# Kernel tuning notes

Hardware: AMD Instinct MI355X
Metric: run time of the kernel (lower is better)

Reference implementation:

```python
import jax, jax.numpy as jnp
import numpy as np

N = 131072

def setup_inputs() -> dict:
    key = jax.random.key(0)
    k_x, k_e, k_w2, k_b2, k_w3, k_b3, k_w4 = jax.random.split(key, 7)
    x = jax.random.randint(k_x, (N, 32), 0, 7424, dtype=jnp.int32)
    emb = jax.random.normal(k_e, (7424, 128), dtype=jnp.float32) * 0.05
    W2 = jax.random.normal(k_w2, (32, 128), dtype=jnp.float32) * 0.05
    b2 = jax.random.normal(k_b2, (32,), dtype=jnp.float32) * 0.05
    W3 = jax.random.normal(k_w3, (32, 64), dtype=jnp.float32) * 0.05
    b3 = jax.random.normal(k_b3, (32,), dtype=jnp.float32) * 0.05
    W4 = jax.random.normal(k_w4, (1, 64), dtype=jnp.float32) * 0.05
    return {"x": x, "emb": emb, "W2": W2, "b2": b2, "W3": W3, "b3": b3, "W4": W4}

def reference(x, emb, W2, b2, W3, b3, W4):
    # x: [N, 32] int indices; use first 29 slots
    idx = x[..., :29]
    h = emb[idx].sum(axis=-2)                    # [N, 128] embedding-bag sum
    h = jax.nn.relu(h)
    h = h @ W2.T + b2                            # [N, 32]
    h = jax.nn.relu(jnp.concatenate((h, -h), axis=-1))   # [N, 64] sign-concat
    h = h @ W3.T + b3                            # [N, 32]
    h = jax.nn.relu(jnp.concatenate((h, -h), axis=-1))   # [N, 64]
    return h @ W4.T                              # [N, 1] (no bias)
```

## Files before the change

kernel.cpp:

```cpp
#include <hip/hip_runtime.h>
#include <hip/hip_fp16.h>


typedef _Float16 h2v_t  __attribute__((ext_vector_type(2)));
typedef _Float16 half8  __attribute__((ext_vector_type(8)));
typedef float    f32x4  __attribute__((ext_vector_type(4)));

constexpr int RPB = 64;

__global__ __launch_bounds__(256) void emb_to_fp16(
    const float* __restrict__ emb, __half2* __restrict__ emb16,
    int npairs_real, int npairs_tot)
{
    int i = blockIdx.x * blockDim.x + threadIdx.x;
    if (i < npairs_tot) {
        float2 v = make_float2(0.f, 0.f);
        if (i < npairs_real) v = ((const float2*)emb)[i];
        emb16[i] = __floats2half2_rn(v.x, v.y);
    }
}

__global__ __launch_bounds__(256) void w_to_fp16(
    const float* __restrict__ W2, const float* __restrict__ W3,
    _Float16* __restrict__ W2h, _Float16* __restrict__ W3h)
{
    int i = blockIdx.x * blockDim.x + threadIdx.x;
    if (i < 4096) W2h[i] = (_Float16)W2[i];
    if (i < 2048) W3h[i] = (_Float16)W3[i];
}

__global__ __launch_bounds__(256, 8) void gather_kernel(
    const int*    __restrict__ x,
    const __half* __restrict__ emb16,
    uint4*        __restrict__ hout,
    int n)
{
    __shared__ int xlds[4][512];

    const int tid  = threadIdx.x;
    const int lane = tid & 63;
    const int wave = tid >> 6;
    const int row0 = blockIdx.x * RPB;
    const int wrow0 = __builtin_amdgcn_readfirstlane(row0 + wave * 16);

    const int g   = lane >> 4;
    const int sub = lane & 15;
    const unsigned subOff = (unsigned)sub * 16u;

    {
        const int4* xb = (const int4*)(x + (size_t)wrow0 * 32);
        int4 a = xb[lane * 2];
        int4 b = xb[lane * 2 + 1];
        if ((lane & 3) == 3) { b.y = 7424; b.z = 7424; b.w = 7424; }
        ((int4*)&xlds[wave][0])[lane * 2]     = a;
        ((int4*)&xlds[wave][0])[lane * 2 + 1] = b;
    }

    #pragma unroll 4
    for (int r = 0; r < 16; ++r) {
        const int* xrow = &xlds[wave][r * 32 + g];
        uint4 v[8];
        #pragma unroll
        for (int b = 0; b < 8; ++b) {
            const int idx = xrow[4 * b];
            const unsigned off = ((unsigned)idx << 8) + subOff;
            v[b] = *(const uint4*)((const char*)emb16 + off);
        }
        h2v_t hacc[4];
        #pragma unroll
        for (int q = 0; q < 4; ++q) hacc[q] = (h2v_t)0;
        #pragma unroll
        for (int b = 0; b < 8; ++b) {
            hacc[0] += __builtin_bit_cast(h2v_t, v[b].x);
            hacc[1] += __builtin_bit_cast(h2v_t, v[b].y);
            hacc[2] += __builtin_bit_cast(h2v_t, v[b].z);
            hacc[3] += __builtin_bit_cast(h2v_t, v[b].w);
        }
        #pragma unroll
        for (int q = 0; q < 4; ++q) {
            unsigned u = __builtin_bit_cast(unsigned, hacc[q]);
            h2v_t t = __builtin_bit_cast(h2v_t, u);
            t += __builtin_bit_cast(h2v_t, (unsigned)__shfl_xor((int)u, 16));
            unsigned u2 = __builtin_bit_cast(unsigned, t);
            t += __builtin_bit_cast(h2v_t, (unsigned)__shfl_xor((int)u2, 32));
            hacc[q] = __builtin_elementwise_max(t, (h2v_t)0);
        }
        if (g == 0) {
            const int row = wrow0 + r;
            if (row < n) {
                uint4 o;
                o.x = __builtin_bit_cast(unsigned, hacc[0]);
                o.y = __builtin_bit_cast(unsigned, hacc[1]);
                o.z = __builtin_bit_cast(unsigned, hacc[2]);
                o.w = __builtin_bit_cast(unsigned, hacc[3]);
                hout[(size_t)row * 16 + sub] = o;
            }
        }
    }
}

__global__ __launch_bounds__(256) void dense_mfma(
    const uint4*    __restrict__ hbuf,
    const _Float16* __restrict__ W2h,
    const _Float16* __restrict__ W3h,
    const float*    __restrict__ b2,
    const float*    __restrict__ b3,
    const float*    __restrict__ W4,
    float*          __restrict__ out, int n)
{
    __shared__ _Float16 a2lds[4][16 * 68];

    const int tid  = threadIdx.x;
    const int lane = tid & 63;
    const int wave = tid >> 6;
    const int q    = lane >> 4;
    const int nn   = lane & 15;
    const int row0 = blockIdx.x * 64 + wave * 16;

    half8 bw2[2][4];
    #pragma unroll
    for (int nt = 0; nt < 2; ++nt)
        #pragma unroll
        for (int kk = 0; kk < 4; ++kk)
            bw2[nt][kk] = __builtin_bit_cast(half8,
                *(const uint4*)((const char*)W2h +
                    ((nt * 16 + nn) * 128 + kk * 32 + q * 8) * 2));

    const int rowm = min(row0 + nn, n - 1);
    const char* hb = (const char*)hbuf + (size_t)rowm * 256;
    half8 af[4];
    #pragma unroll
    for (int kk = 0; kk < 4; ++kk)
        af[kk] = __builtin_bit_cast(half8,
            *(const uint4*)(hb + kk * 64 + q * 16));

    f32x4 acc0 = {0.f, 0.f, 0.f, 0.f}, acc1 = {0.f, 0.f, 0.f, 0.f};
    #pragma unroll
    for (int kk = 0; kk < 4; ++kk) {
        acc0 = __builtin_amdgcn_mfma_f32_16x16x32_f16(af[kk], bw2[0][kk], acc0, 0, 0, 0);
        acc1 = __builtin_amdgcn_mfma_f32_16x16x32_f16(af[kk], bw2[1][kk], acc1, 0, 0, 0);
    }
    const float bb0 = b2[nn], bb1 = b2[16 + nn];

    _Float16* a2 = &a2lds[wave][0];
    #pragma unroll
    for (int r = 0; r < 4; ++r) {
        const float v0 = acc0[r] + bb0;
        const float v1 = acc1[r] + bb1;
        const int m = q * 4 + r;
        a2[m * 68 + nn]      = (_Float16)fmaxf(v0, 0.f);
        a2[m * 68 + 16 + nn] = (_Float16)fmaxf(v1, 0.f);
        a2[m * 68 + 32 + nn] = (_Float16)fmaxf(-v0, 0.f);
        a2[m * 68 + 48 + nn] = (_Float16)fmaxf(-v1, 0.f);
    }

    half8 bw3[2][2];
    #pragma unroll
    for (int nt = 0; nt < 2; ++nt)
        #pragma unroll
        for (int kk = 0; kk < 2; ++kk)
            bw3[nt][kk] = __builtin_bit_cast(half8,
                *(const uint4*)((const char*)W3h +
                    ((nt * 16 + nn) * 64 + kk * 32 + q * 8) * 2));

    half8 a2f[2];
    #pragma unroll
    for (int kk = 0; kk < 2; ++kk) {
        const _Float16* p = &a2[nn * 68 + kk * 32 + q * 8];
        half8 t;
        #pragma unroll
        for (int j = 0; j < 8; ++j) t[j] = p[j];
        a2f[kk] = t;
    }

    f32x4 acc30 = {0.f, 0.f, 0.f, 0.f}, acc31 = {0.f, 0.f, 0.f, 0.f};
    #pragma unroll
    for (int kk = 0; kk < 2; ++kk) {
        acc30 = __builtin_amdgcn_mfma_f32_16x16x32_f16(a2f[kk], bw3[0][kk], acc30, 0, 0, 0);
        acc31 = __builtin_amdgcn_mfma_f32_16x16x32_f16(a2f[kk], bw3[1][kk], acc31, 0, 0, 0);
    }
    const float bb30 = b3[nn], bb31 = b3[16 + nn];

    const float w4a = W4[nn],      w4b = W4[16 + nn];
    const float w4c = W4[32 + nn], w4d = W4[48 + nn];
    float o[4];
    #pragma unroll
    for (int r = 0; r < 4; ++r) {
        const float v0 = acc30[r] + bb30;
        const float v1 = acc31[r] + bb31;
        o[r] = fmaxf(v0, 0.f) * w4a + fmaxf(-v0, 0.f) * w4c
             + fmaxf(v1, 0.f) * w4b + fmaxf(-v1, 0.f) * w4d;
    }
    #pragma unroll
    for (int s = 1; s < 16; s <<= 1) {
        #pragma unroll
        for (int r = 0; r < 4; ++r) o[r] += __shfl_xor(o[r], s);
    }
    if (nn == 0) {
        #pragma unroll
        for (int r = 0; r < 4; ++r) {
            const int row = row0 + q * 4 + r;
            if (row < n) out[row] = o[r];
        }
    }
}

__global__ __launch_bounds__(256) void nnue_fused(
    const int*    __restrict__ x,
    const __half* __restrict__ emb16,
    const float*  __restrict__ W2, const float* __restrict__ b2,
    const float*  __restrict__ W3, const float* __restrict__ b3,
    const float*  __restrict__ W4,
    float*        __restrict__ out, int n)
{
    __shared__ int     xlds[4][512];
    __shared__ __half2 hbuf[64][65];
    __shared__ float   h2T[32 * 64];
    __shared__ float   obuf[4][64];

    const int tid  = threadIdx.x;
    const int lane = tid & 63;
    const int wave = tid >> 6;
    const int row0 = blockIdx.x * RPB;
    const int wrow0 = __builtin_amdgcn_readfirstlane(row0 + wave * 16);
    const int g   = lane >> 4;
    const int sub = lane & 15;
    const unsigned subOff = (unsigned)sub * 16u;

    {
        const int4* xb = (const int4*)(x + (size_t)wrow0 * 32);
        int4 a = xb[lane * 2];
        int4 b = xb[lane * 2 + 1];
        if ((lane & 3) == 3) { b.y = 7424; b.z = 7424; b.w = 7424; }
        ((int4*)&xlds[wave][0])[lane * 2]     = a;
        ((int4*)&xlds[wave][0])[lane * 2 + 1] = b;
    }

    #pragma unroll 4
    for (int r = 0; r < 16; ++r) {
        const int* xrow = &xlds[wave][r * 32 + g];
        uint4 v[8];
        #pragma unroll
        for (int b = 0; b < 8; ++b) {
            const int idx = xrow[4 * b];
            const unsigned off = ((unsigned)idx << 8) + subOff;
            v[b] = *(const uint4*)((const char*)emb16 + off);
        }
        h2v_t hacc[4];
        #pragma unroll
        for (int q = 0; q < 4; ++q) hacc[q] = (h2v_t)0;
        #pragma unroll
        for (int b = 0; b < 8; ++b) {
            hacc[0] += __builtin_bit_cast(h2v_t, v[b].x);
            hacc[1] += __builtin_bit_cast(h2v_t, v[b].y);
            hacc[2] += __builtin_bit_cast(h2v_t, v[b].z);
            hacc[3] += __builtin_bit_cast(h2v_t, v[b].w);
        }
        #pragma unroll
        for (int q = 0; q < 4; ++q) {
            unsigned u = __builtin_bit_cast(unsigned, hacc[q]);
            h2v_t t = __builtin_bit_cast(h2v_t, u);
            t += __builtin_bit_cast(h2v_t, (unsigned)__shfl_xor((int)u, 16));
            unsigned u2 = __builtin_bit_cast(unsigned, t);
            t += __builtin_bit_cast(h2v_t, (unsigned)__shfl_xor((int)u2, 32));
            hacc[q] = __builtin_elementwise_max(t, (h2v_t)0);
        }
        if (g == 0) {
            const int row = wave * 16 + r;
            #pragma unroll
            for (int q = 0; q < 4; ++q)
                hbuf[row][sub * 4 + q] = __builtin_bit_cast(__half2, hacc[q]);
        }
    }
    __syncthreads();

    {
        const int j0 = wave * 8;
        const int rr = lane;
        float acc[8];
        #pragma unroll
        for (int j = 0; j < 8; ++j) acc[j] = b2[j0 + j];
        #pragma unroll
        for (int d2 = 0; d2 < 64; ++d2) {
            const __half2 hv = hbuf[rr][d2];
            const float vx = __low2float(hv), vy = __high2float(hv);
            #pragma unroll
            for (int j = 0; j < 8; ++j) {
                const float* w = W2 + (size_t)(j0 + j) * 128 + d2 * 2;
                acc[j] = fmaf(vx, w[0], acc[j]);
                acc[j] = fmaf(vy, w[1], acc[j]);
            }
        }
        #pragma unroll
        for (int j = 0; j < 8; ++j) h2T[(j0 + j) * 64 + rr] = acc[j];
    }
    __syncthreads();

    {
        const int j0 = wave * 8;
        const int rr = lane;
        float h2v[32];
        #pragma unroll
        for (int k = 0; k < 32; ++k) h2v[k] = h2T[k * 64 + rr];
        float acc[8];
        #pragma unroll
        for (int j = 0; j < 8; ++j) acc[j] = b3[j0 + j];
        #pragma unroll
        for (int k = 0; k < 32; ++k) {
            const float p = fmaxf(h2v[k], 0.f);
            const float m = fmaxf(-h2v[k], 0.f);
            #pragma unroll
            for (int j = 0; j < 8; ++j) {
                const float* w = W3 + (size_t)(j0 + j) * 64;
                acc[j] = fmaf(p, w[k],      acc[j]);
                acc[j] = fmaf(m, w[32 + k], acc[j]);
            }
        }
        float o = 0.f;
        #pragma unroll
        for (int j = 0; j < 8; ++j) {
            const int jj = j0 + j;
            o = fmaf(fmaxf(acc[j], 0.f),  W4[jj],      o);
            o = fmaf(fmaxf(-acc[j], 0.f), W4[32 + jj], o);
        }
        obuf[wave][rr] = o;
    }
    __syncthreads();

    if (tid < 64) {
        const int row = row0 + tid;
        if (row < n)
            out[row] = obuf[0][tid] + obuf[1][tid] + obuf[2][tid] + obuf[3][tid];
    }
}

extern "C" void kernel_launch(void* const* d_in, const int* in_sizes, int n_in,
                              void* d_out, int out_size, void* d_ws, size_t ws_size,
                              hipStream_t stream) {
    const int*   x   = (const int*)  d_in[0];
    const float* emb = (const float*)d_in[1];
    const float* W2  = (const float*)d_in[2];
    const float* b2  = (const float*)d_in[3];
    const float* W3  = (const float*)d_in[4];
    const float* b3  = (const float*)d_in[5];
    const float* W4  = (const float*)d_in[6];
    float* out = (float*)d_out;
    const int n = out_size;

    __half2* emb16 = (__half2*)d_ws;
    const int npairs_real = 7424 * 64;
    const int npairs_tot  = 7425 * 64;
    hipLaunchKernelGGL(emb_to_fp16, dim3((npairs_tot + 255) / 256), dim3(256),
                       0, stream, emb, emb16, npairs_real, npairs_tot);

    const size_t emb_bytes = (size_t)7425 * 256;
    const size_t w2h_off   = emb_bytes;
    const size_t w3h_off   = w2h_off + 8192;
    const size_t h_off     = w3h_off + 4096;
    const size_t h_bytes   = (size_t)n * 256;
    const bool   split_ok  = ws_size >= h_off + h_bytes;

    if (split_ok) {
        _Float16* W2h = (_Float16*)((char*)d_ws + w2h_off);
        _Float16* W3h = (_Float16*)((char*)d_ws + w3h_off);
        uint4*    hb  = (uint4*)   ((char*)d_ws + h_off);
        hipLaunchKernelGGL(w_to_fp16, dim3(16), dim3(256), 0, stream,
                           W2, W3, W2h, W3h);
        hipLaunchKernelGGL(gather_kernel, dim3((n + RPB - 1) / RPB), dim3(256),
                           0, stream, x, (const __half*)emb16, hb, n);
        hipLaunchKernelGGL(dense_mfma, dim3((n + 63) / 64), dim3(256),
                           0, stream, (const uint4*)hb, W2h, W3h, b2, b3, W4,
                           out, n);
    } else {
        hipLaunchKernelGGL(nnue_fused, dim3((n + RPB - 1) / RPB), dim3(256),
                           0, stream, x, (const __half*)emb16, W2, b2, W3, b3,
                           W4, out, n);
    }
}
```

Baseline: 131.9 us.

## Fuse embedding gather and MFMA dense layers into one kernel via LDS

Merges the gather kernel and the dense MFMA kernel into a single kernel. Each wave keeps its 16 pooled fp16 rows in a padded LDS tile and feeds them straight to the MFMA layers, so the N×256-byte intermediate buffer is never written to or read back from global memory, and one launch is removed. The index scratch space is reused for the second-layer activations. Occupancy drops from 8 to 6 blocks per CU, and the dense phase now sits in the same kernel as the latency-bound gather, which may hurt overlap.

```diff
diff --git a/kernel.cpp b/kernel.cpp
--- a/kernel.cpp
+++ b/kernel.cpp
@@ -29,13 +29,18 @@
     if (i < 2048) W3h[i] = (_Float16)W3[i];
 }
 
-__global__ __launch_bounds__(256, 8) void gather_kernel(
-    const int*    __restrict__ x,
-    const __half* __restrict__ emb16,
-    uint4*        __restrict__ hout,
-    int n)
+__global__ __launch_bounds__(256, 6) void nnue_one(
+    const int*      __restrict__ x,
+    const __half*   __restrict__ emb16,
+    const _Float16* __restrict__ W2h,
+    const _Float16* __restrict__ W3h,
+    const float*    __restrict__ b2,
+    const float*    __restrict__ b3,
+    const float*    __restrict__ W4,
+    float*          __restrict__ out, int n)
 {
-    __shared__ int xlds[4][512];
+    __shared__ uint4 hT[4][16 * 17];
+    __shared__ __align__(16) char scratch[4][2176];
 
     const int tid  = threadIdx.x;
     const int lane = tid & 63;
@@ -47,18 +52,20 @@
     const int sub = lane & 15;
     const unsigned subOff = (unsigned)sub * 16u;
 
+    int* xw = (int*)&scratch[wave][0];
+
     {
         const int4* xb = (const int4*)(x + (size_t)wrow0 * 32);
         int4 a = xb[lane * 2];
         int4 b = xb[lane * 2 + 1];
         if ((lane & 3) == 3) { b.y = 7424; b.z = 7424; b.w = 7424; }
-        ((int4*)&xlds[wave][0])[lane * 2]     = a;
-        ((int4*)&xlds[wave][0])[lane * 2 + 1] = b;
+        ((int4*)xw)[lane * 2]     = a;
+        ((int4*)xw)[lane * 2 + 1] = b;
     }
 
     #pragma unroll 4
     for (int r = 0; r < 16; ++r) {
-        const int* xrow = &xlds[wave][r * 32 + g];
+        const int* xrow = &xw[r * 32 + g];
         uint4 v[8];
         #pragma unroll
         for (int b = 0; b < 8; ++b) {
@@ -86,36 +93,17 @@
             hacc[q] = __builtin_elementwise_max(t, (h2v_t)0);
         }
         if (g == 0) {
-            const int row = wrow0 + r;
-            if (row < n) {
-                uint4 o;
-                o.x = __builtin_bit_cast(unsigned, hacc[0]);
-                o.y = __builtin_bit_cast(unsigned, hacc[1]);
-                o.z = __builtin_bit_cast(unsigned, hacc[2]);
-                o.w = __builtin_bit_cast(unsigned, hacc[3]);
-                hout[(size_t)row * 16 + sub] = o;
-            }
-        }
-    }
-}
-
-__global__ __launch_bounds__(256) void dense_mfma(
-    const uint4*    __restrict__ hbuf,
-    const _Float16* __restrict__ W2h,
-    const _Float16* __restrict__ W3h,
-    const float*    __restrict__ b2,
-    const float*    __restrict__ b3,
-    const float*    __restrict__ W4,
-    float*          __restrict__ out, int n)
-{
-    __shared__ _Float16 a2lds[4][16 * 68];
-
-    const int tid  = threadIdx.x;
-    const int lane = tid & 63;
-    const int wave = tid >> 6;
-    const int q    = lane >> 4;
-    const int nn   = lane & 15;
-    const int row0 = blockIdx.x * 64 + wave * 16;
+            uint4 o;
+            o.x = __builtin_bit_cast(unsigned, hacc[0]);
+            o.y = __builtin_bit_cast(unsigned, hacc[1]);
+            o.z = __builtin_bit_cast(unsigned, hacc[2]);
+            o.w = __builtin_bit_cast(unsigned, hacc[3]);
+            hT[wave][r * 17 + sub] = o;
+        }
+    }
+
+    const int q  = lane >> 4;
+    const int nn = lane & 15;
 
     half8 bw2[2][4];
     #pragma unroll
@@ -126,13 +114,10 @@
                 *(const uint4*)((const char*)W2h +
                     ((nt * 16 + nn) * 128 + kk * 32 + q * 8) * 2));
 
-    const int rowm = min(row0 + nn, n - 1);
-    const char* hb = (const char*)hbuf + (size_t)rowm * 256;
     half8 af[4];
     #pragma unroll
     for (int kk = 0; kk < 4; ++kk)
-        af[kk] = __builtin_bit_cast(half8,
-            *(const uint4*)(hb + kk * 64 + q * 16));
+        af[kk] = __builtin_bit_cast(half8, hT[wave][nn * 17 + (4 * kk + q)]);
 
     f32x4 acc0 = {0.f, 0.f, 0.f, 0.f}, acc1 = {0.f, 0.f, 0.f, 0.f};
     #pragma unroll
@@ -142,7 +127,7 @@
     }
     const float bb0 = b2[nn], bb1 = b2[16 + nn];
 
-    _Float16* a2 = &a2lds[wave][0];
+    _Float16* a2 = (_Float16*)&scratch[wave][0];
     #pragma unroll
     for (int r = 0; r < 4; ++r) {
         const float v0 = acc0[r] + bb0;
@@ -199,7 +184,7 @@
     if (nn == 0) {
         #pragma unroll
         for (int r = 0; r < 4; ++r) {
-            const int row = row0 + q * 4 + r;
+            const int row = wrow0 + q * 4 + r;
             if (row < n) out[row] = o[r];
         }
     }
@@ -356,21 +341,17 @@
     const size_t emb_bytes = (size_t)7425 * 256;
     const size_t w2h_off   = emb_bytes;
     const size_t w3h_off   = w2h_off + 8192;
-    const size_t h_off     = w3h_off + 4096;
-    const size_t h_bytes   = (size_t)n * 256;
-    const bool   split_ok  = ws_size >= h_off + h_bytes;
-
-    if (split_ok) {
+    const size_t need      = w3h_off + 4096;
+    const bool   fused_ok  = ws_size >= need;
+
+    if (fused_ok) {
         _Float16* W2h = (_Float16*)((char*)d_ws + w2h_off);
         _Float16* W3h = (_Float16*)((char*)d_ws + w3h_off);
-        uint4*    hb  = (uint4*)   ((char*)d_ws + h_off);
         hipLaunchKernelGGL(w_to_fp16, dim3(16), dim3(256), 0, stream,
                            W2, W3, W2h, W3h);
-        hipLaunchKernelGGL(gather_kernel, dim3((n + RPB - 1) / RPB), dim3(256),
-                           0, stream, x, (const __half*)emb16, hb, n);
-        hipLaunchKernelGGL(dense_mfma, dim3((n + 63) / 64), dim3(256),
-                           0, stream, (const uint4*)hb, W2h, W3h, b2, b3, W4,
-                           out, n);
+        hipLaunchKernelGGL(nnue_one, dim3((n + RPB - 1) / RPB), dim3(256),
+                           0, stream, x, (const __half*)emb16, W2h, W3h,
+                           b2, b3, W4, out, n);
     } else {
         hipLaunchKernelGGL(nnue_fused, dim3((n + RPB - 1) / RPB), dim3(256),
                            0, stream, x, (const __half*)emb16, W2, b2, W3, b3,
```

After: 121.6 us. 1.09x faster.
